# Optimization experiments

Measured on AMD Instinct MI355X. Metric: run time of the kernel, lower is better.

The kernel has to match this reference:

```python
import jax, jax.numpy as jnp
import numpy as np

B, K_KNOW, D = 16, 8192, 128


def setup_inputs() -> dict:
    key = jax.random.key(0)
    ks = jax.random.split(key, 8)
    scale1 = np.sqrt(6.0 / (D + D)).astype(np.float32)   # glorot_uniform for (d,d)
    scale2 = np.sqrt(6.0 / (2 * D + D)).astype(np.float32)  # glorot_uniform for (2d,d)
    return {
        "c_cur": jax.random.normal(ks[0], (B, D), dtype=jnp.float32),
        "m_prev": jax.random.normal(ks[1], (B, D), dtype=jnp.float32),
        "knowledge": jax.random.normal(ks[2], (B, K_KNOW, D), dtype=jnp.float32),
        "im_kernel": jax.random.uniform(ks[3], (D, D), jnp.float32, -scale1, scale1),
        "ik_kernel": jax.random.uniform(ks[4], (D, D), jnp.float32, -scale1, scale1),
        "id_kernel": jax.random.uniform(ks[5], (2 * D, D), jnp.float32, -scale2, scale2),
        "ra_kernel": jax.random.uniform(ks[6], (D, D), jnp.float32, -scale1, scale1),
        "im_bias": jnp.zeros((D,), jnp.float32),
        "ik_bias": jnp.zeros((D,), jnp.float32),
        "id_bias": jnp.zeros((D,), jnp.float32),
        "ra_bias": jnp.zeros((D,), jnp.float32),
    }


def reference(c_cur, m_prev, knowledge,
              im_kernel, ik_kernel, id_kernel, ra_kernel,
              im_bias, ik_bias, id_bias, ra_bias):
    # Im: [B, 1, d] ; Ik: [B, K, d]
    Im = (m_prev @ im_kernel + im_bias)[:, None, :]
    Ik = jnp.einsum('bkd,de->bke', knowledge, ik_kernel) + ik_bias
    I = Im * Ik                                            # [B, K, d]
    Id = jnp.einsum('bkf,fe->bke',
                    jnp.concatenate([I, knowledge], axis=-1),
                    id_kernel) + id_bias                   # [B, K, d]
    cI = c_cur[:, None, :] * Id                            # [B, K, d]
    ra = jnp.einsum('bkd,de->bke', cI, ra_kernel) + ra_bias
    rv = jax.nn.softmax(ra, axis=1)                        # softmax over knowledge axis
    r = jnp.sum(rv * knowledge, axis=1)                    # [B, d]
    return r
```

## Files before the change

kernel.cpp:

```cpp
#include <hip/hip_runtime.h>
#include <cmath>


#define B_ 16
#define K_ 8192
#define D_ 128
#define CK 128
#define NCHUNK (K_ / CK)
#define TR 32
#define NT (CK / TR)
#define LDP 136

typedef __attribute__((ext_vector_type(8))) short short8;
typedef __attribute__((ext_vector_type(4))) float f32x4;

__device__ __forceinline__ unsigned short f2bf(float x) {
  unsigned int u = __float_as_uint(x);
  u = (u + 0x7fffu + ((u >> 16) & 1u)) >> 16;
  return (unsigned short)u;
}
__device__ __forceinline__ float bf2f(unsigned short h) {
  return __uint_as_float(((unsigned int)h) << 16);
}

__global__ void pack_weights(const float* __restrict__ Wik,
                             const float* __restrict__ Wid,
                             const float* __restrict__ Wra,
                             unsigned short* __restrict__ packed) {
  const int F = blockIdx.x;
  const int l = threadIdx.x;
  const int h = F & 1;
  const int n = (F >> 1) & 7;
  const int QQ = F >> 4;
  const float* W; int q;
  if (QQ < 4)       { W = Wik; q = QQ; }
  else if (QQ < 12) { W = Wid; q = QQ - 4; }
  else              { W = Wra; q = QQ - 12; }
  const int col = n * 16 + (l & 15);
  const int kb = q * 32 + (l >> 4) * 8;
  unsigned short* dst = packed + (size_t)F * 512 + l * 8;
#pragma unroll
  for (int j = 0; j < 8; ++j) {
    const float v = W[(kb + j) * D_ + col];
    const unsigned short hi = f2bf(v);
    dst[j] = h ? f2bf(v - bf2f(hi)) : hi;
  }
}

__global__ void im_proj_kernel(const float* __restrict__ m_prev,
                               const float* __restrict__ Wim,
                               const float* __restrict__ bim,
                               float* __restrict__ Im) {
  const int b = blockIdx.x;
  const int e = threadIdx.x;
  const float* mp = m_prev + b * D_;
  float acc = 0.f;
#pragma unroll 8
  for (int d = 0; d < D_; ++d) acc = fmaf(mp[d], Wim[d * D_ + e], acc);
  Im[b * D_ + e] = acc + bim[e];
}

__global__ __launch_bounds__(256, 2) void readunit_main(
    const float* __restrict__ c_cur,
    const float* __restrict__ knowledge,
    const float* __restrict__ bik,
    const float* __restrict__ bid,
    const float* __restrict__ bra,
    const float* __restrict__ Im,
    const unsigned short* __restrict__ packed,
    float* __restrict__ partial) {
  __shared__ unsigned short know_h[CK * LDP];
  __shared__ unsigned short I_h[CK * LDP];

  const int chunk = blockIdx.x;
  const int b = blockIdx.y;
  const int tid = threadIdx.x;
  const int lane = tid & 63;
  const int wn = tid >> 6;
  const int lr = lane & 15;
  const int lg = lane >> 4;

  const float* gk = knowledge + ((size_t)b * K_ + (size_t)chunk * CK) * D_;
#pragma unroll
  for (int i = 0; i < 16; ++i) {
    const int flat = tid + 256 * i;
    const int row = flat >> 5;
    const int c4 = (flat & 31) * 4;
    const float4 v = *(const float4*)(gk + row * D_ + c4);
    ushort4 hv;
    hv.x = f2bf(v.x); hv.y = f2bf(v.y); hv.z = f2bf(v.z); hv.w = f2bf(v.w);
    *(ushort4*)(&know_h[row * LDP + c4]) = hv;
  }

  float imv[2], cv[2], bikv[2], bidv[2], brav[2];
#pragma unroll
  for (int f = 0; f < 2; ++f) {
    const int col = wn * 32 + f * 16 + lr;
    imv[f]  = Im[b * D_ + col];
    cv[f]   = c_cur[b * D_ + col];
    bikv[f] = bik[col];
    bidv[f] = bid[col];
    brav[f] = bra[col];
  }
  __syncthreads();

  short8 Bf[2][8][2];

#pragma unroll
  for (int q = 0; q < 4; ++q)
#pragma unroll
    for (int f = 0; f < 2; ++f)
#pragma unroll
      for (int h = 0; h < 2; ++h) {
        const int F = (q * 8 + (wn * 2 + f)) * 2 + h;
        Bf[f][q][h] = *(const short8*)(packed + (size_t)F * 512 + lane * 8);
      }
  for (int t = 0; t < NT; ++t) {
    const int rb = t * TR;
    f32x4 acc[2][2] = {};
#pragma unroll
    for (int q = 0; q < 4; ++q) {
      const short8 a0 = *(const short8*)(&know_h[(rb + lr) * LDP + q * 32 + lg * 8]);
      const short8 a1 = *(const short8*)(&know_h[(rb + 16 + lr) * LDP + q * 32 + lg * 8]);
#pragma unroll
      for (int f = 0; f < 2; ++f) {
        acc[0][f] = __builtin_amdgcn_mfma_f32_16x16x32_bf16(a0, Bf[f][q][0], acc[0][f], 0, 0, 0);
        acc[0][f] = __builtin_amdgcn_mfma_f32_16x16x32_bf16(a0, Bf[f][q][1], acc[0][f], 0, 0, 0);
        acc[1][f] = __builtin_amdgcn_mfma_f32_16x16x32_bf16(a1, Bf[f][q][0], acc[1][f], 0, 0, 0);
        acc[1][f] = __builtin_amdgcn_mfma_f32_16x16x32_bf16(a1, Bf[f][q][1], acc[1][f], 0, 0, 0);
      }
    }
#pragma unroll
    for (int m = 0; m < 2; ++m)
#pragma unroll
      for (int f = 0; f < 2; ++f) {
        const int col = wn * 32 + f * 16 + lr;
#pragma unroll
        for (int r = 0; r < 4; ++r) {
          const int row = rb + m * 16 + lg * 4 + r;
          I_h[row * LDP + col] = f2bf((acc[m][f][r] + bikv[f]) * imv[f]);
        }
      }
  }
  __syncthreads();

#pragma unroll
  for (int q = 0; q < 8; ++q)
#pragma unroll
    for (int f = 0; f < 2; ++f)
#pragma unroll
      for (int h = 0; h < 2; ++h) {
        const int F = ((4 + q) * 8 + (wn * 2 + f)) * 2 + h;
        Bf[f][q][h] = *(const short8*)(packed + (size_t)F * 512 + lane * 8);
      }
  for (int t = 0; t < NT; ++t) {
    const int rb = t * TR;
    f32x4 acc[2][2] = {};
#pragma unroll
    for (int q = 0; q < 8; ++q) {
      const unsigned short* src = (q < 4)
          ? &I_h[(rb + lr) * LDP + q * 32 + lg * 8]
          : &know_h[(rb + lr) * LDP + (q - 4) * 32 + lg * 8];
      const short8 a0 = *(const short8*)(src);
      const short8 a1 = *(const short8*)(src + 16 * LDP);
#pragma unroll
      for (int f = 0; f < 2; ++f) {
        acc[0][f] = __builtin_amdgcn_mfma_f32_16x16x32_bf16(a0, Bf[f][q][0], acc[0][f], 0, 0, 0);
        acc[0][f] = __builtin_amdgcn_mfma_f32_16x16x32_bf16(a0, Bf[f][q][1], acc[0][f], 0, 0, 0);
        acc[1][f] = __builtin_amdgcn_mfma_f32_16x16x32_bf16(a1, Bf[f][q][0], acc[1][f], 0, 0, 0);
        acc[1][f] = __builtin_amdgcn_mfma_f32_16x16x32_bf16(a1, Bf[f][q][1], acc[1][f], 0, 0, 0);
      }
    }
    __syncthreads();
#pragma unroll
    for (int m = 0; m < 2; ++m)
#pragma unroll
      for (int f = 0; f < 2; ++f) {
        const int col = wn * 32 + f * 16 + lr;
#pragma unroll
        for (int r = 0; r < 4; ++r) {
          const int row = rb + m * 16 + lg * 4 + r;
          I_h[row * LDP + col] = f2bf(cv[f] * (acc[m][f][r] + bidv[f]));
        }
      }
  }
  __syncthreads();

#pragma unroll
  for (int q = 0; q < 4; ++q)
#pragma unroll
    for (int f = 0; f < 2; ++f)
#pragma unroll
      for (int h = 0; h < 2; ++h) {
        const int F = ((12 + q) * 8 + (wn * 2 + f)) * 2 + h;
        Bf[f][q][h] = *(const short8*)(packed + (size_t)F * 512 + lane * 8);
      }
  float sm[2] = {-1e30f, -1e30f}, sl[2] = {0.f, 0.f}, sacc[2] = {0.f, 0.f};
  for (int t = 0; t < NT; ++t) {
    const int rb = t * TR;
    f32x4 acc[2][2] = {};
#pragma unroll
    for (int q = 0; q < 4; ++q) {
      const short8 a0 = *(const short8*)(&I_h[(rb + lr) * LDP + q * 32 + lg * 8]);
      const short8 a1 = *(const short8*)(&I_h[(rb + 16 + lr) * LDP + q * 32 + lg * 8]);
#pragma unroll
      for (int f = 0; f < 2; ++f) {
        acc[0][f] = __builtin_amdgcn_mfma_f32_16x16x32_bf16(a0, Bf[f][q][0], acc[0][f], 0, 0, 0);
        acc[0][f] = __builtin_amdgcn_mfma_f32_16x16x32_bf16(a0, Bf[f][q][1], acc[0][f], 0, 0, 0);
        acc[1][f] = __builtin_amdgcn_mfma_f32_16x16x32_bf16(a1, Bf[f][q][0], acc[1][f], 0, 0, 0);
        acc[1][f] = __builtin_amdgcn_mfma_f32_16x16x32_bf16(a1, Bf[f][q][1], acc[1][f], 0, 0, 0);
      }
    }
#pragma unroll
    for (int f = 0; f < 2; ++f) {
      const int col = wn * 32 + f * 16 + lr;
      float v[8];
#pragma unroll
      for (int m = 0; m < 2; ++m)
#pragma unroll
        for (int r = 0; r < 4; ++r) v[m * 4 + r] = acc[m][f][r] + brav[f];
      float tmax = v[0];
#pragma unroll
      for (int i = 1; i < 8; ++i) tmax = fmaxf(tmax, v[i]);
      const float mnew = fmaxf(sm[f], tmax);
      const float scale = __expf(sm[f] - mnew);
      sl[f] *= scale;
      sacc[f] *= scale;
#pragma unroll
      for (int m = 0; m < 2; ++m)
#pragma unroll
        for (int r = 0; r < 4; ++r) {
          const int row = rb + m * 16 + lg * 4 + r;
          const float p = __expf(v[m * 4 + r] - mnew);
          sl[f] += p;
          sacc[f] = fmaf(p, bf2f(know_h[row * LDP + col]), sacc[f]);
        }
      sm[f] = mnew;
    }
  }

#pragma unroll
  for (int f = 0; f < 2; ++f) {
#pragma unroll
    for (int s = 0; s < 2; ++s) {
      const int off = (s == 0) ? 16 : 32;
      const float om = __shfl_xor(sm[f], off);
      const float ol = __shfl_xor(sl[f], off);
      const float oa = __shfl_xor(sacc[f], off);
      const float mn = fmaxf(sm[f], om);
      const float e0 = __expf(sm[f] - mn), e1 = __expf(om - mn);
      sl[f] = sl[f] * e0 + ol * e1;
      sacc[f] = sacc[f] * e0 + oa * e1;
      sm[f] = mn;
    }
  }
  if (lg == 0) {
    float* p = partial + (size_t)(b * NCHUNK + chunk) * (3 * D_);
#pragma unroll
    for (int f = 0; f < 2; ++f) {
      const int col = wn * 32 + f * 16 + lr;
      p[col] = sm[f];
      p[D_ + col] = sl[f];
      p[2 * D_ + col] = sacc[f];
    }
  }
}

__global__ void readunit_reduce(const float* __restrict__ partial,
                                float* __restrict__ out) {
  const int b = blockIdx.x;
  const int d = threadIdx.x;
  float m = -1e30f, l = 0.f, a = 0.f;
  for (int c = 0; c < NCHUNK; ++c) {
    const float* p = partial + (size_t)(b * NCHUNK + c) * (3 * D_);
    const float mc = p[d], lc = p[D_ + d], ac = p[2 * D_ + d];
    const float mn = fmaxf(m, mc);
    const float s0 = __expf(m - mn), s1 = __expf(mc - mn);
    l = l * s0 + lc * s1;
    a = a * s0 + ac * s1;
    m = mn;
  }
  out[b * D_ + d] = a / l;
}

extern "C" void kernel_launch(void* const* d_in, const int* in_sizes, int n_in,
                              void* d_out, int out_size, void* d_ws, size_t ws_size,
                              hipStream_t stream) {
  const float* c_cur = (const float*)d_in[0];
  const float* m_prev = (const float*)d_in[1];
  const float* knowledge = (const float*)d_in[2];
  const float* Wim = (const float*)d_in[3];
  const float* Wik = (const float*)d_in[4];
  const float* Wid = (const float*)d_in[5];
  const float* Wra = (const float*)d_in[6];
  const float* bim = (const float*)d_in[7];
  const float* bik = (const float*)d_in[8];
  const float* bid = (const float*)d_in[9];
  const float* bra = (const float*)d_in[10];
  float* out = (float*)d_out;

  float* Im = (float*)d_ws;
  float* partial = Im + B_ * D_;
  unsigned short* packed =
      (unsigned short*)(partial + (size_t)B_ * NCHUNK * 3 * D_);

  pack_weights<<<256, 64, 0, stream>>>(Wik, Wid, Wra, packed);
  im_proj_kernel<<<B_, D_, 0, stream>>>(m_prev, Wim, bim, Im);
  readunit_main<<<dim3(NCHUNK, B_), 256, 0, stream>>>(
      c_cur, knowledge, bik, bid, bra, Im, packed, partial);
  readunit_reduce<<<B_, D_, 0, stream>>>(partial, out);
}
```

Baseline: 161.1 us.

## Process chunks in 64-row passes, raise occupancy, merge prep kernels, parallelize reduce

The main kernel now processes each 128-row chunk in two 64-row passes. This halves LDS usage per block, and the launch bounds are raised to 4 blocks per CU to get more occupancy. The weight-packing and Im projection kernels are merged into one launch, and the final reduce splits the chunk loop across 4 thread groups combined through shared memory. The cost is reloading the packed weight fragments from global memory on every pass and adding extra barriers, and the tighter register budget may cause spills.

```diff
diff --git a/kernel.cpp b/kernel.cpp
--- a/kernel.cpp
+++ b/kernel.cpp
@@ -7,8 +7,10 @@
 #define D_ 128
 #define CK 128
 #define NCHUNK (K_ / CK)
-#define TR 32
-#define NT (CK / TR)
+#define SUB 64
+#define NPASS (CK / SUB)
+#define TRS 32
+#define NTS (SUB / TRS)
 #define LDP 136
 
 typedef __attribute__((ext_vector_type(8))) short short8;
@@ -23,44 +25,47 @@
   return __uint_as_float(((unsigned int)h) << 16);
 }
 
-__global__ void pack_weights(const float* __restrict__ Wik,
-                             const float* __restrict__ Wid,
-                             const float* __restrict__ Wra,
-                             unsigned short* __restrict__ packed) {
-  const int F = blockIdx.x;
+__global__ void prep_kernel(const float* __restrict__ m_prev,
+                            const float* __restrict__ Wim,
+                            const float* __restrict__ bim,
+                            const float* __restrict__ Wik,
+                            const float* __restrict__ Wid,
+                            const float* __restrict__ Wra,
+                            unsigned short* __restrict__ packed,
+                            float* __restrict__ Im) {
+  const int blk = blockIdx.x;
   const int l = threadIdx.x;
-  const int h = F & 1;
-  const int n = (F >> 1) & 7;
-  const int QQ = F >> 4;
-  const float* W; int q;
-  if (QQ < 4)       { W = Wik; q = QQ; }
-  else if (QQ < 12) { W = Wid; q = QQ - 4; }
-  else              { W = Wra; q = QQ - 12; }
-  const int col = n * 16 + (l & 15);
-  const int kb = q * 32 + (l >> 4) * 8;
-  unsigned short* dst = packed + (size_t)F * 512 + l * 8;
-#pragma unroll
-  for (int j = 0; j < 8; ++j) {
-    const float v = W[(kb + j) * D_ + col];
-    const unsigned short hi = f2bf(v);
-    dst[j] = h ? f2bf(v - bf2f(hi)) : hi;
-  }
-}
-
-__global__ void im_proj_kernel(const float* __restrict__ m_prev,
-                               const float* __restrict__ Wim,
-                               const float* __restrict__ bim,
-                               float* __restrict__ Im) {
-  const int b = blockIdx.x;
-  const int e = threadIdx.x;
-  const float* mp = m_prev + b * D_;
-  float acc = 0.f;
+  if (blk < 256) {
+    const int F = blk;
+    const int h = F & 1;
+    const int n = (F >> 1) & 7;
+    const int QQ = F >> 4;
+    const float* W; int q;
+    if (QQ < 4)       { W = Wik; q = QQ; }
+    else if (QQ < 12) { W = Wid; q = QQ - 4; }
+    else              { W = Wra; q = QQ - 12; }
+    const int col = n * 16 + (l & 15);
+    const int kb = q * 32 + (l >> 4) * 8;
+    unsigned short* dst = packed + (size_t)F * 512 + l * 8;
+#pragma unroll
+    for (int j = 0; j < 8; ++j) {
+      const float v = W[(kb + j) * D_ + col];
+      const unsigned short hi = f2bf(v);
+      dst[j] = h ? f2bf(v - bf2f(hi)) : hi;
+    }
+  } else {
+    const int idx = blk - 256;
+    const int b = idx >> 1;
+    const int e = (idx & 1) * 64 + l;
+    const float* mp = m_prev + b * D_;
+    float acc = 0.f;
 #pragma unroll 8
-  for (int d = 0; d < D_; ++d) acc = fmaf(mp[d], Wim[d * D_ + e], acc);
-  Im[b * D_ + e] = acc + bim[e];
-}
-
-__global__ __launch_bounds__(256, 2) void readunit_main(
+    for (int d = 0; d < D_; ++d) acc = fmaf(mp[d], Wim[d * D_ + e], acc);
+    Im[b * D_ + e] = acc + bim[e];
+  }
+}
+
+__global__ __launch_bounds__(256, 4) void readunit_main(
     const float* __restrict__ c_cur,
     const float* __restrict__ knowledge,
     const float* __restrict__ bik,
@@ -69,8 +74,8 @@
     const float* __restrict__ Im,
     const unsigned short* __restrict__ packed,
     float* __restrict__ partial) {
-  __shared__ unsigned short know_h[CK * LDP];
-  __shared__ unsigned short I_h[CK * LDP];
+  __shared__ unsigned short know_h[SUB * LDP];
+  __shared__ unsigned short I_h[SUB * LDP];
 
   const int chunk = blockIdx.x;
   const int b = blockIdx.y;
@@ -80,18 +85,6 @@
   const int lr = lane & 15;
   const int lg = lane >> 4;
 
-  const float* gk = knowledge + ((size_t)b * K_ + (size_t)chunk * CK) * D_;
-#pragma unroll
-  for (int i = 0; i < 16; ++i) {
-    const int flat = tid + 256 * i;
-    const int row = flat >> 5;
-    const int c4 = (flat & 31) * 4;
-    const float4 v = *(const float4*)(gk + row * D_ + c4);
-    ushort4 hv;
-    hv.x = f2bf(v.x); hv.y = f2bf(v.y); hv.z = f2bf(v.z); hv.w = f2bf(v.w);
-    *(ushort4*)(&know_h[row * LDP + c4]) = hv;
-  }
-
   float imv[2], cv[2], bikv[2], bidv[2], brav[2];
 #pragma unroll
   for (int f = 0; f < 2; ++f) {
@@ -102,140 +95,157 @@
     bidv[f] = bid[col];
     brav[f] = bra[col];
   }
-  __syncthreads();
 
   short8 Bf[2][8][2];
-
-#pragma unroll
-  for (int q = 0; q < 4; ++q)
-#pragma unroll
-    for (int f = 0; f < 2; ++f)
-#pragma unroll
-      for (int h = 0; h < 2; ++h) {
-        const int F = (q * 8 + (wn * 2 + f)) * 2 + h;
-        Bf[f][q][h] = *(const short8*)(packed + (size_t)F * 512 + lane * 8);
+  float sm[2] = {-1e30f, -1e30f}, sl[2] = {0.f, 0.f}, sacc[2] = {0.f, 0.f};
+
+  for (int pass = 0; pass < NPASS; ++pass) {
+    __syncthreads();
+
+    const float* gk = knowledge +
+        ((size_t)b * K_ + (size_t)(chunk * CK + pass * SUB)) * D_;
+#pragma unroll
+    for (int i = 0; i < 8; ++i) {
+      const int flat = tid + 256 * i;
+      const int row = flat >> 5;
+      const int c4 = (flat & 31) * 4;
+      const float4 v = *(const float4*)(gk + row * D_ + c4);
+      ushort4 hv;
+      hv.x = f2bf(v.x); hv.y = f2bf(v.y); hv.z = f2bf(v.z); hv.w = f2bf(v.w);
+      *(ushort4*)(&know_h[row * LDP + c4]) = hv;
+    }
+    __syncthreads();
+
+#pragma unroll
+    for (int q = 0; q < 4; ++q)
+#pragma unroll
+      for (int f = 0; f < 2; ++f)
+#pragma unroll
+        for (int h = 0; h < 2; ++h) {
+          const int F = (q * 8 + (wn * 2 + f)) * 2 + h;
+          Bf[f][q][h] = *(const short8*)(packed + (size_t)F * 512 + lane * 8);
+        }
+    for (int t = 0; t < NTS; ++t) {
+      const int rb = t * TRS;
+      f32x4 acc[2][2] = {};
+#pragma unroll
+      for (int q = 0; q < 4; ++q) {
+        const short8 a0 = *(const short8*)(&know_h[(rb + lr) * LDP + q * 32 + lg * 8]);
+        const short8 a1 = *(const short8*)(&know_h[(rb + 16 + lr) * LDP + q * 32 + lg * 8]);
+#pragma unroll
+        for (int f = 0; f < 2; ++f) {
+          acc[0][f] = __builtin_amdgcn_mfma_f32_16x16x32_bf16(a0, Bf[f][q][0], acc[0][f], 0, 0, 0);
+          acc[0][f] = __builtin_amdgcn_mfma_f32_16x16x32_bf16(a0, Bf[f][q][1], acc[0][f], 0, 0, 0);
+          acc[1][f] = __builtin_amdgcn_mfma_f32_16x16x32_bf16(a1, Bf[f][q][0], acc[1][f], 0, 0, 0);
+          acc[1][f] = __builtin_amdgcn_mfma_f32_16x16x32_bf16(a1, Bf[f][q][1], acc[1][f], 0, 0, 0);
+        }
       }
-  for (int t = 0; t < NT; ++t) {
-    const int rb = t * TR;
-    f32x4 acc[2][2] = {};
-#pragma unroll
-    for (int q = 0; q < 4; ++q) {
-      const short8 a0 = *(const short8*)(&know_h[(rb + lr) * LDP + q * 32 + lg * 8]);
-      const short8 a1 = *(const short8*)(&know_h[(rb + 16 + lr) * LDP + q * 32 + lg * 8]);
-#pragma unroll
-      for (int f = 0; f < 2; ++f) {
-        acc[0][f] = __builtin_amdgcn_mfma_f32_16x16x32_bf16(a0, Bf[f][q][0], acc[0][f], 0, 0, 0);
-        acc[0][f] = __builtin_amdgcn_mfma_f32_16x16x32_bf16(a0, Bf[f][q][1], acc[0][f], 0, 0, 0);
-        acc[1][f] = __builtin_amdgcn_mfma_f32_16x16x32_bf16(a1, Bf[f][q][0], acc[1][f], 0, 0, 0);
-        acc[1][f] = __builtin_amdgcn_mfma_f32_16x16x32_bf16(a1, Bf[f][q][1], acc[1][f], 0, 0, 0);
+#pragma unroll
+      for (int m = 0; m < 2; ++m)
+#pragma unroll
+        for (int f = 0; f < 2; ++f) {
+          const int col = wn * 32 + f * 16 + lr;
+#pragma unroll
+          for (int r = 0; r < 4; ++r) {
+            const int row = rb + m * 16 + lg * 4 + r;
+            I_h[row * LDP + col] = f2bf((acc[m][f][r] + bikv[f]) * imv[f]);
+          }
+        }
+    }
+    __syncthreads();
+
+#pragma unroll
+    for (int q = 0; q < 8; ++q)
+#pragma unroll
+      for (int f = 0; f < 2; ++f)
+#pragma unroll
+        for (int h = 0; h < 2; ++h) {
+          const int F = ((4 + q) * 8 + (wn * 2 + f)) * 2 + h;
+          Bf[f][q][h] = *(const short8*)(packed + (size_t)F * 512 + lane * 8);
+        }
+    for (int t = 0; t < NTS; ++t) {
+      const int rb = t * TRS;
+      f32x4 acc[2][2] = {};
+#pragma unroll
+      for (int q = 0; q < 8; ++q) {
+        const unsigned short* src = (q < 4)
+            ? &I_h[(rb + lr) * LDP + q * 32 + lg * 8]
+            : &know_h[(rb + lr) * LDP + (q - 4) * 32 + lg * 8];
+        const short8 a0 = *(const short8*)(src);
+        const short8 a1 = *(const short8*)(src + 16 * LDP);
+#pragma unroll
+        for (int f = 0; f < 2; ++f) {
+          acc[0][f] = __builtin_amdgcn_mfma_f32_16x16x32_bf16(a0, Bf[f][q][0], acc[0][f], 0, 0, 0);
+          acc[0][f] = __builtin_amdgcn_mfma_f32_16x16x32_bf16(a0, Bf[f][q][1], acc[0][f], 0, 0, 0);
+          acc[1][f] = __builtin_amdgcn_mfma_f32_16x16x32_bf16(a1, Bf[f][q][0], acc[1][f], 0, 0, 0);
+          acc[1][f] = __builtin_amdgcn_mfma_f32_16x16x32_bf16(a1, Bf[f][q][1], acc[1][f], 0, 0, 0);
+        }
       }
-    }
-#pragma unroll
-    for (int m = 0; m < 2; ++m)
+      __syncthreads();
+#pragma unroll
+      for (int m = 0; m < 2; ++m)
+#pragma unroll
+        for (int f = 0; f < 2; ++f) {
+          const int col = wn * 32 + f * 16 + lr;
+#pragma unroll
+          for (int r = 0; r < 4; ++r) {
+            const int row = rb + m * 16 + lg * 4 + r;
+            I_h[row * LDP + col] = f2bf(cv[f] * (acc[m][f][r] + bidv[f]));
+          }
+        }
+    }
+    __syncthreads();
+
+#pragma unroll
+    for (int q = 0; q < 4; ++q)
+#pragma unroll
+      for (int f = 0; f < 2; ++f)
+#pragma unroll
+        for (int h = 0; h < 2; ++h) {
+          const int F = ((12 + q) * 8 + (wn * 2 + f)) * 2 + h;
+          Bf[f][q][h] = *(const short8*)(packed + (size_t)F * 512 + lane * 8);
+        }
+    for (int t = 0; t < NTS; ++t) {
+      const int rb = t * TRS;
+      f32x4 acc[2][2] = {};
+#pragma unroll
+      for (int q = 0; q < 4; ++q) {
+        const short8 a0 = *(const short8*)(&I_h[(rb + lr) * LDP + q * 32 + lg * 8]);
+        const short8 a1 = *(const short8*)(&I_h[(rb + 16 + lr) * LDP + q * 32 + lg * 8]);
+#pragma unroll
+        for (int f = 0; f < 2; ++f) {
+          acc[0][f] = __builtin_amdgcn_mfma_f32_16x16x32_bf16(a0, Bf[f][q][0], acc[0][f], 0, 0, 0);
+          acc[0][f] = __builtin_amdgcn_mfma_f32_16x16x32_bf16(a0, Bf[f][q][1], acc[0][f], 0, 0, 0);
+          acc[1][f] = __builtin_amdgcn_mfma_f32_16x16x32_bf16(a1, Bf[f][q][0], acc[1][f], 0, 0, 0);
+          acc[1][f] = __builtin_amdgcn_mfma_f32_16x16x32_bf16(a1, Bf[f][q][1], acc[1][f], 0, 0, 0);
+        }
+      }
 #pragma unroll
       for (int f = 0; f < 2; ++f) {
         const int col = wn * 32 + f * 16 + lr;
-#pragma unroll
-        for (int r = 0; r < 4; ++r) {
-          const int row = rb + m * 16 + lg * 4 + r;
-          I_h[row * LDP + col] = f2bf((acc[m][f][r] + bikv[f]) * imv[f]);
-        }
+        float v[8];
+#pragma unroll
+        for (int m = 0; m < 2; ++m)
+#pragma unroll
+          for (int r = 0; r < 4; ++r) v[m * 4 + r] = acc[m][f][r] + brav[f];
+        float tmax = v[0];
+#pragma unroll
+        for (int i = 1; i < 8; ++i) tmax = fmaxf(tmax, v[i]);
+        const float mnew = fmaxf(sm[f], tmax);
+        const float scale = __expf(sm[f] - mnew);
+        sl[f] *= scale;
+        sacc[f] *= scale;
+#pragma unroll
+        for (int m = 0; m < 2; ++m)
+#pragma unroll
+          for (int r = 0; r < 4; ++r) {
+            const int row = rb + m * 16 + lg * 4 + r;
+            const float p = __expf(v[m * 4 + r] - mnew);
+            sl[f] += p;
+            sacc[f] = fmaf(p, bf2f(know_h[row * LDP + col]), sacc[f]);
+          }
+        sm[f] = mnew;
       }
-  }
-  __syncthreads();
-
-#pragma unroll
-  for (int q = 0; q < 8; ++q)
-#pragma unroll
-    for (int f = 0; f < 2; ++f)
-#pragma unroll
-      for (int h = 0; h < 2; ++h) {
-        const int F = ((4 + q) * 8 + (wn * 2 + f)) * 2 + h;
-        Bf[f][q][h] = *(const short8*)(packed + (size_t)F * 512 + lane * 8);
-      }
-  for (int t = 0; t < NT; ++t) {
-    const int rb = t * TR;
-    f32x4 acc[2][2] = {};
-#pragma unroll
-    for (int q = 0; q < 8; ++q) {
-      const unsigned short* src = (q < 4)
-          ? &I_h[(rb + lr) * LDP + q * 32 + lg * 8]
-          : &know_h[(rb + lr) * LDP + (q - 4) * 32 + lg * 8];
-      const short8 a0 = *(const short8*)(src);
-      const short8 a1 = *(const short8*)(src + 16 * LDP);
-#pragma unroll
-      for (int f = 0; f < 2; ++f) {
-        acc[0][f] = __builtin_amdgcn_mfma_f32_16x16x32_bf16(a0, Bf[f][q][0], acc[0][f], 0, 0, 0);
-        acc[0][f] = __builtin_amdgcn_mfma_f32_16x16x32_bf16(a0, Bf[f][q][1], acc[0][f], 0, 0, 0);
-        acc[1][f] = __builtin_amdgcn_mfma_f32_16x16x32_bf16(a1, Bf[f][q][0], acc[1][f], 0, 0, 0);
-        acc[1][f] = __builtin_amdgcn_mfma_f32_16x16x32_bf16(a1, Bf[f][q][1], acc[1][f], 0, 0, 0);
-      }
-    }
-    __syncthreads();
-#pragma unroll
-    for (int m = 0; m < 2; ++m)
-#pragma unroll
-      for (int f = 0; f < 2; ++f) {
-        const int col = wn * 32 + f * 16 + lr;
-#pragma unroll
-        for (int r = 0; r < 4; ++r) {
-          const int row = rb + m * 16 + lg * 4 + r;
-          I_h[row * LDP + col] = f2bf(cv[f] * (acc[m][f][r] + bidv[f]));
-        }
-      }
-  }
-  __syncthreads();
-
-#pragma unroll
-  for (int q = 0; q < 4; ++q)
-#pragma unroll
-    for (int f = 0; f < 2; ++f)
-#pragma unroll
-      for (int h = 0; h < 2; ++h) {
-        const int F = ((12 + q) * 8 + (wn * 2 + f)) * 2 + h;
-        Bf[f][q][h] = *(const short8*)(packed + (size_t)F * 512 + lane * 8);
-      }
-  float sm[2] = {-1e30f, -1e30f}, sl[2] = {0.f, 0.f}, sacc[2] = {0.f, 0.f};
-  for (int t = 0; t < NT; ++t) {
-    const int rb = t * TR;
-    f32x4 acc[2][2] = {};
-#pragma unroll
-    for (int q = 0; q < 4; ++q) {
-      const short8 a0 = *(const short8*)(&I_h[(rb + lr) * LDP + q * 32 + lg * 8]);
-      const short8 a1 = *(const short8*)(&I_h[(rb + 16 + lr) * LDP + q * 32 + lg * 8]);
-#pragma unroll
-      for (int f = 0; f < 2; ++f) {
-        acc[0][f] = __builtin_amdgcn_mfma_f32_16x16x32_bf16(a0, Bf[f][q][0], acc[0][f], 0, 0, 0);
-        acc[0][f] = __builtin_amdgcn_mfma_f32_16x16x32_bf16(a0, Bf[f][q][1], acc[0][f], 0, 0, 0);
-        acc[1][f] = __builtin_amdgcn_mfma_f32_16x16x32_bf16(a1, Bf[f][q][0], acc[1][f], 0, 0, 0);
-        acc[1][f] = __builtin_amdgcn_mfma_f32_16x16x32_bf16(a1, Bf[f][q][1], acc[1][f], 0, 0, 0);
-      }
-    }
-#pragma unroll
-    for (int f = 0; f < 2; ++f) {
-      const int col = wn * 32 + f * 16 + lr;
-      float v[8];
-#pragma unroll
-      for (int m = 0; m < 2; ++m)
-#pragma unroll
-        for (int r = 0; r < 4; ++r) v[m * 4 + r] = acc[m][f][r] + brav[f];
-      float tmax = v[0];
-#pragma unroll
-      for (int i = 1; i < 8; ++i) tmax = fmaxf(tmax, v[i]);
-      const float mnew = fmaxf(sm[f], tmax);
-      const float scale = __expf(sm[f] - mnew);
-      sl[f] *= scale;
-      sacc[f] *= scale;
-#pragma unroll
-      for (int m = 0; m < 2; ++m)
-#pragma unroll
-        for (int r = 0; r < 4; ++r) {
-          const int row = rb + m * 16 + lg * 4 + r;
-          const float p = __expf(v[m * 4 + r] - mnew);
-          sl[f] += p;
-          sacc[f] = fmaf(p, bf2f(know_h[row * LDP + col]), sacc[f]);
-        }
-      sm[f] = mnew;
     }
   }
 
@@ -268,10 +278,13 @@
 
 __global__ void readunit_reduce(const float* __restrict__ partial,
                                 float* __restrict__ out) {
+  __shared__ float s_m[4][D_], s_l[4][D_], s_a[4][D_];
   const int b = blockIdx.x;
-  const int d = threadIdx.x;
+  const int tid = threadIdx.x;
+  const int g = tid >> 7;
+  const int d = tid & 127;
   float m = -1e30f, l = 0.f, a = 0.f;
-  for (int c = 0; c < NCHUNK; ++c) {
+  for (int c = g * 16; c < g * 16 + 16; ++c) {
     const float* p = partial + (size_t)(b * NCHUNK + c) * (3 * D_);
     const float mc = p[d], lc = p[D_ + d], ac = p[2 * D_ + d];
     const float mn = fmaxf(m, mc);
@@ -280,7 +293,20 @@
     a = a * s0 + ac * s1;
     m = mn;
   }
-  out[b * D_ + d] = a / l;
+  s_m[g][d] = m; s_l[g][d] = l; s_a[g][d] = a;
+  __syncthreads();
+  if (g == 0) {
+#pragma unroll
+    for (int i = 1; i < 4; ++i) {
+      const float mc = s_m[i][d], lc = s_l[i][d], ac = s_a[i][d];
+      const float mn = fmaxf(m, mc);
+      const float s0 = __expf(m - mn), s1 = __expf(mc - mn);
+      l = l * s0 + lc * s1;
+      a = a * s0 + ac * s1;
+      m = mn;
+    }
+    out[b * D_ + d] = a / l;
+  }
 }
 
 extern "C" void kernel_launch(void* const* d_in, const int* in_sizes, int n_in,
@@ -304,9 +330,8 @@
   unsigned short* packed =
       (unsigned short*)(partial + (size_t)B_ * NCHUNK * 3 * D_);
 
-  pack_weights<<<256, 64, 0, stream>>>(Wik, Wid, Wra, packed);
-  im_proj_kernel<<<B_, D_, 0, stream>>>(m_prev, Wim, bim, Im);
+  prep_kernel<<<288, 64, 0, stream>>>(m_prev, Wim, bim, Wik, Wid, Wra, packed, Im);
   readunit_main<<<dim3(NCHUNK, B_), 256, 0, stream>>>(
       c_cur, knowledge, bik, bid, bra, Im, packed, partial);
-  readunit_reduce<<<B_, D_, 0, stream>>>(partial, out);
-}
+  readunit_reduce<<<B_, 512, 0, stream>>>(partial, out);
+}
```

Result: slower. 345.7 us (+114.6%).
